# Kernel tuning notes

Measured on AMD Instinct MI355X. Metric: run time of the kernel, lower is better.

Reference implementation:

```python
import jax, jax.numpy as jnp
import numpy as np

B, S, T = 16, 256, 2048
V, D, H, L, FF, NM = 3000, 512, 8, 6, 2048, 80
DH = D // H


def _make_pe(max_len=5000, d=D):
    pos = np.arange(max_len, dtype=np.float32)[:, None]
    div = np.exp(np.arange(0, d, 2, dtype=np.float32) * (-np.log(10000.0) / d))
    pe = np.zeros((max_len, d), dtype=np.float32)
    pe[:, 0::2] = np.sin(pos * div)
    pe[:, 1::2] = np.cos(pos * div)
    return jnp.asarray(pe[None])  # [1, max_len, D]


def setup_inputs() -> dict:
    key = jax.random.key(0)
    ks = jax.random.split(key, 24)
    f = jnp.float32
    n = lambda k, sh, s=0.02: jax.random.normal(k, sh, f) * s
    return {
        'text_ids': jax.random.randint(ks[0], (B, S), 0, V),
        'text_lengths': jax.random.randint(ks[1], (B,), S // 2, S + 1),
        'mel_targets': jax.random.normal(ks[2], (B, NM, T), f),
        'emb': n(ks[3], (V, D), 0.05),
        'pe': _make_pe(),
        'Wqkv': n(ks[4], (L, D, 3 * D)), 'bqkv': jnp.zeros((L, 3 * D), f),
        'Wo': n(ks[5], (L, D, D)), 'bo': jnp.zeros((L, D), f),
        'ln1_s': jnp.ones((L, D), f), 'ln1_b': jnp.zeros((L, D), f),
        'ln2_s': jnp.ones((L, D), f), 'ln2_b': jnp.zeros((L, D), f),
        'W1': n(ks[6], (L, D, FF)), 'b1': jnp.zeros((L, FF), f),
        'W2': n(ks[7], (L, FF, D)), 'b2': jnp.zeros((L, D), f),
        'mel_W1': n(ks[8], (D, FF)), 'mel_b1': jnp.zeros((FF,), f),
        'mel_W2': n(ks[9], (FF, NM)), 'mel_b2': jnp.zeros((NM,), f),
        'dur_W1': n(ks[10], (D, 256)), 'dur_b1': jnp.zeros((256,), f),
        'dur_W2': n(ks[11], (256, 1)), 'dur_b2': jnp.zeros((1,), f),
    }


def _layer_norm(x, s, b, eps=1e-5):
    m = jnp.mean(x, -1, keepdims=True)
    v = jnp.mean(jnp.square(x - m), -1, keepdims=True)
    return (x - m) * jax.lax.rsqrt(v + eps) * s + b


def _length_regulate(enc, durations, target_len):
    # enc [B,S,D], durations [B,S] -> [B,target_len,D]
    dur = jnp.maximum(jnp.round(durations).astype(jnp.int32), 1)
    cum = jnp.cumsum(dur, axis=1)                              # [B,S] inclusive
    pos = jnp.arange(target_len)                               # [T]
    idx = jnp.sum(pos[None, None, :] >= cum[:, :, None], axis=1)  # [B,T]
    idx = jnp.minimum(idx, enc.shape[1] - 1)
    valid = pos[None, :] < cum[:, -1:]                         # [B,T]
    out = jnp.take_along_axis(enc, idx[..., None], axis=1)
    return out * valid[..., None].astype(enc.dtype)


def reference(text_ids, text_lengths, mel_targets, emb, pe, Wqkv, bqkv, Wo, bo,
              ln1_s, ln1_b, ln2_s, ln2_b, W1, b1, W2, b2,
              mel_W1, mel_b1, mel_W2, mel_b2, dur_W1, dur_b1, dur_W2, dur_b2):
    x = emb[text_ids] + pe[:, :S]                              # [B,S,D]
    pad = jnp.arange(S)[None, :] >= text_lengths[:, None]      # True = padded key
    bias = jnp.where(pad, -1e9, 0.0)[:, None, None, :]         # [B,1,1,S]
    scale = 1.0 / jnp.sqrt(jnp.float32(DH))
    for l in range(L):
        qkv = x @ Wqkv[l] + bqkv[l]
        q, k, v = jnp.split(qkv, 3, axis=-1)
        q = q.reshape(B, S, H, DH).transpose(0, 2, 1, 3)
        k = k.reshape(B, S, H, DH).transpose(0, 2, 1, 3)
        v = v.reshape(B, S, H, DH).transpose(0, 2, 1, 3)
        scores = jnp.einsum('bhqd,bhkd->bhqk', q, k) * scale + bias
        attn = jax.nn.softmax(scores, axis=-1)
        o = jnp.einsum('bhqk,bhkd->bhqd', attn, v)
        o = o.transpose(0, 2, 1, 3).reshape(B, S, D) @ Wo[l] + bo[l]
        x = _layer_norm(x + o, ln1_s[l], ln1_b[l])              # post-LN (torch default)
        ff = jax.nn.relu(x @ W1[l] + b1[l]) @ W2[l] + b2[l]
        x = _layer_norm(x + ff, ln2_s[l], ln2_b[l])
    enc = x
    dur_h = jax.nn.relu(enc @ dur_W1 + dur_b1)
    durations = jax.nn.softplus((dur_h @ dur_W2 + dur_b2).squeeze(-1))  # [B,S]
    target_len = mel_targets.shape[2]
    expanded = _length_regulate(enc, durations, target_len)    # [B,T,D]
    mel = jax.nn.relu(expanded @ mel_W1 + mel_b1) @ mel_W2 + mel_b2
    mel = mel.transpose(0, 2, 1)                               # [B,NM,T]
    return mel, durations, enc
```

## Files before the change

### kernel.cpp

```cpp
#include <hip/hip_runtime.h>
#include <math.h>

#define B_ 16
#define S_ 256
#define T_ 2048
#define D_ 512
#define H_ 8
#define L_ 6
#define FF_ 2048
#define NM_ 80
#define M_ 4096

typedef float floatx4 __attribute__((ext_vector_type(4)));
typedef __bf16 bf16x8 __attribute__((ext_vector_type(8)));

__device__ __forceinline__ float bf2f(unsigned u) {
    return __uint_as_float((u & 0xffffu) << 16);
}
__device__ __forceinline__ unsigned short f2bf(float f) {
    unsigned u = __float_as_uint(f);
    unsigned r = u + 0x7fffu + ((u >> 16) & 1u);
    return (unsigned short)(r >> 16);
}
__device__ __forceinline__ void gload_lds16(const void* g, void* l) {
    __builtin_amdgcn_global_load_lds(
        (const __attribute__((address_space(1))) void*)g,
        (__attribute__((address_space(3))) void*)l, 16, 0, 0);
}

__device__ __forceinline__ void tr_body(
    const float* __restrict__ src, unsigned short* __restrict__ dst,
    int K, int N, int bx, int by, int bz, float (*tile)[33], int Ns )
{
    const int k0 = by * 32, n0 = bx * 32;
    src += (size_t)bz * K * Ns;
    dst += (size_t)bz * K * N;
    const int tid = threadIdx.x;
    const int tx = tid & 31, ty = tid >> 5;
#pragma unroll
    for (int i = 0; i < 32; i += 8) {
        int n = n0 + tx;
        tile[ty + i][tx] = (n < Ns) ? src[(size_t)(k0 + ty + i) * Ns + n] : 0.f;
    }
    __syncthreads();
#pragma unroll
    for (int i = 0; i < 32; i += 8)
        dst[(size_t)(n0 + ty + i) * K + k0 + tx] = f2bf(tile[tx][ty + i]);
}

__global__ __launch_bounds__(256) void prep_weights(
    const float* __restrict__ Wqkv, const float* __restrict__ Wo,
    const float* __restrict__ W1, const float* __restrict__ W2,
    const float* __restrict__ melW1, const float* __restrict__ melW2,
    const float* __restrict__ durW1, const float* __restrict__ melb1,
    const float* __restrict__ melb2, const float* __restrict__ durb1,
    unsigned short* __restrict__ Wqkv_t, unsigned short* __restrict__ Wo_t,
    unsigned short* __restrict__ W1_t, unsigned short* __restrict__ W2_t,
    unsigned short* __restrict__ wcomb, unsigned short* __restrict__ melW2_t,
    float* __restrict__ cbias, float* __restrict__ c0)
{
    __shared__ float tile[32][33];
    int bid = blockIdx.x;
    if (bid < 4608) {
        int z = bid / 768, r = bid % 768;
        tr_body(Wqkv, Wqkv_t, 512, 1536, r % 48, r / 48, z, tile, 1536);
        return;
    }
    bid -= 4608;
    if (bid < 1536) {
        int z = bid / 256, r = bid % 256;
        tr_body(Wo, Wo_t, 512, 512, r % 16, r / 16, z, tile, 512);
        return;
    }
    bid -= 1536;
    if (bid < 6144) {
        int z = bid / 1024, r = bid % 1024;
        tr_body(W1, W1_t, 512, 2048, r % 64, r / 64, z, tile, 2048);
        return;
    }
    bid -= 6144;
    if (bid < 6144) {
        int z = bid / 1024, r = bid % 1024;
        tr_body(W2, W2_t, 2048, 512, r % 16, r / 16, z, tile, 512);
        return;
    }
    bid -= 6144;
    if (bid < 1024) {
        tr_body(melW1, wcomb, 512, 2304, bid % 64, bid / 64, 0, tile, 2048);
        return;
    }
    bid -= 1024;
    if (bid < 256) {
        tr_body(melW2, melW2_t, 2048, 128, bid % 4, bid / 4, 0, tile, 80);
        return;
    }
    bid -= 256;
    if (bid < 128) {
        tr_body(durW1, wcomb + (size_t)2048 * 512, 512, 256, bid % 8, bid / 8, 0, tile, 256);
        return;
    }
    bid -= 128;
    if (bid < 9) {
        int idx = bid * 256 + threadIdx.x;
        cbias[idx] = (idx < 2048) ? melb1[idx] : durb1[idx - 2048];
        return;
    }
    bid -= 9;
    {
        float* red = (float*)tile;
        const int c = bid;
        const int tid = threadIdx.x;
        float p = 0.f;
        for (int f = tid; f < 2048; f += 256)
            p += fmaxf(melb1[f], 0.f) * melW2[(size_t)f * 80 + c];
#pragma unroll
        for (int off = 32; off >= 1; off >>= 1) p += __shfl_xor(p, off, 64);
        if ((tid & 63) == 0) red[tid >> 6] = p;
        __syncthreads();
        if (tid == 0) c0[c] = red[0] + red[1] + red[2] + red[3] + melb2[c];
    }
}

__global__ __launch_bounds__(128) void embed_bf16(
    const int* __restrict__ ids, const float* __restrict__ emb,
    const float* __restrict__ pe, unsigned short* __restrict__ x)
{
    const int r = blockIdx.x;
    const int c = threadIdx.x * 4;
    const int id = ids[r];
    const int s = r & (S_ - 1);
    float4 e = *(const float4*)(emb + (size_t)id * D_ + c);
    float4 p = *(const float4*)(pe + (size_t)s * D_ + c);
    ushort4 o;
    o.x = f2bf(e.x + p.x); o.y = f2bf(e.y + p.y);
    o.z = f2bf(e.z + p.z); o.w = f2bf(e.w + p.w);
    *(ushort4*)(x + (size_t)r * D_ + c) = o;
}

template<int BM, int BN>
__global__ __launch_bounds__(256) void gemm2(
    const unsigned short* __restrict__ A, const unsigned short* __restrict__ Bt,
    const float* __restrict__ bias, unsigned short* __restrict__ Cb,
    float* __restrict__ Cpart, unsigned short* __restrict__ vtp,
    int N, int klen, int act, int lda)
{
    constexpr int NSUB_A = BM / 8;
    constexpr int NSUB_B = BN / 8;
    constexpr int NSUB = NSUB_A + NSUB_B;
    constexpr int NL = NSUB / 4;
    constexpr int BUFSZ = NSUB * 1024;
    constexpr int AOFF = NSUB_A * 1024;
    constexpr int WM = BM / 32, WN = BN / 32;
    __shared__ __attribute__((aligned(16))) char smem[2 * BUFSZ];

    const int tid = threadIdx.x;
    const int wave = tid >> 6, lane = tid & 63;
    const int lm = lane & 15, quad = lane >> 4;
    const int wm = wave >> 1, wn = wave & 1;
    const int m0 = blockIdx.y * BM;
    const int n0 = blockIdx.x * BN;
    const int Kfull = klen * gridDim.z;
    const int kb = blockIdx.z * klen;

    floatx4 acc[WM][WN];
#pragma unroll
    for (int i = 0; i < WM; i++)
#pragma unroll
        for (int j = 0; j < WN; j++) acc[i][j] = (floatx4){0.f, 0.f, 0.f, 0.f};

    const unsigned short* ga[NL];
    int loff[NL];
#pragma unroll
    for (int j = 0; j < NL; j++) {
        int sid = wave * NL + j;
        if (sid < NSUB_A) {
            int mi = sid >> 1, ki = sid & 1;
            ga[j] = A + (size_t)(m0 + mi * 16 + lm) * lda + kb + ki * 32 + quad * 8;
            loff[j] = sid * 1024;
        } else {
            int t = sid - NSUB_A;
            int ni = t >> 1, ki = t & 1;
            ga[j] = Bt + (size_t)(n0 + ni * 16 + lm) * Kfull + kb + ki * 32 + quad * 8;
            loff[j] = AOFF + t * 1024;
        }
    }

#pragma unroll
    for (int j = 0; j < NL; j++) gload_lds16(ga[j], smem + loff[j]);

    for (int kt = 0; kt < klen; kt += 64) {
        char* sc = smem + ((kt >> 6) & 1) * BUFSZ;
        if (kt + 64 < klen) {
            char* sn = smem + (((kt >> 6) + 1) & 1) * BUFSZ;
#pragma unroll
            for (int j = 0; j < NL; j++) gload_lds16(ga[j] + kt + 64, sn + loff[j]);
            __builtin_amdgcn_s_waitcnt(0x0F70 | NL);
        } else {
            __builtin_amdgcn_s_waitcnt(0x0F70);
        }
        asm volatile("" ::: "memory");
        __builtin_amdgcn_s_barrier();
        asm volatile("" ::: "memory");

#pragma unroll
        for (int ki = 0; ki < 2; ki++) {
            bf16x8 af[WM], bfr[WN];
#pragma unroll
            for (int i = 0; i < WM; i++)
                af[i] = *(const bf16x8*)(sc + ((((wm * WM + i) * 2 + ki) << 10) + (lane << 4)));
#pragma unroll
            for (int j = 0; j < WN; j++)
                bfr[j] = *(const bf16x8*)(sc + AOFF + ((((wn * WN + j) * 2 + ki) << 10) + (lane << 4)));
#pragma unroll
            for (int i = 0; i < WM; i++)
#pragma unroll
                for (int j = 0; j < WN; j++)
                    acc[i][j] = __builtin_amdgcn_mfma_f32_16x16x32_bf16(
                        af[i], bfr[j], acc[i][j], 0, 0, 0);
        }
        asm volatile("" ::: "memory");
        __builtin_amdgcn_s_barrier();
        asm volatile("" ::: "memory");
    }

    if constexpr (BM == 128 && BN == 128) {
        if (vtp != nullptr && n0 >= 1024) {
            unsigned short* sT = (unsigned short*)smem;
#pragma unroll
            for (int mi = 0; mi < WM; mi++) {
                const int rl = wm * 64 + mi * 16 + quad * 4;
#pragma unroll
                for (int nj = 0; nj < WN; nj++) {
                    const int cl = wn * 64 + nj * 16 + lm;
                    const float bv = bias[n0 + cl];
                    ushort4 t4;
                    t4.x = f2bf(acc[mi][nj][0] + bv);
                    t4.y = f2bf(acc[mi][nj][1] + bv);
                    t4.z = f2bf(acc[mi][nj][2] + bv);
                    t4.w = f2bf(acc[mi][nj][3] + bv);
                    *(ushort4*)(sT + cl * 136 + rl) = t4;
                }
            }
            __syncthreads();
            const int b = m0 >> 8;
            const int s0 = m0 & 255;
            const int h0 = (n0 - 1024) >> 6;
#pragma unroll
            for (int i = 0; i < 8; i++) {
                int idx = i * 256 + tid;
                int d = idx >> 4, c = idx & 15;
                uint4 v = *(const uint4*)(sT + d * 136 + c * 8);
                int bh = b * 8 + h0 + (d >> 6);
                *(uint4*)(vtp + ((size_t)bh * 64 + (d & 63)) * 256 + s0 + c * 8) = v;
            }
            return;
        }
    }

    if (gridDim.z == 1) {
#pragma unroll
        for (int mi = 0; mi < WM; mi++) {
            const int rb = m0 + wm * (WM * 16) + mi * 16 + quad * 4;
#pragma unroll
            for (int nj = 0; nj < WN; nj++) {
                const int col = n0 + wn * (WN * 16) + nj * 16 + lm;
                const float bv = bias[col];
#pragma unroll
                for (int r = 0; r < 4; r++) {
                    float o = acc[mi][nj][r] + bv;
                    if (act) o = fmaxf(o, 0.f);
                    Cb[(size_t)(rb + r) * N + col] = f2bf(o);
                }
            }
        }
    } else {
        float* Cp = Cpart + (size_t)blockIdx.z * gridDim.y * BM * N;
#pragma unroll
        for (int mi = 0; mi < WM; mi++) {
            const int rb = m0 + wm * (WM * 16) + mi * 16 + quad * 4;
#pragma unroll
            for (int nj = 0; nj < WN; nj++) {
                const int col = n0 + wn * (WN * 16) + nj * 16 + lm;
#pragma unroll
                for (int r = 0; r < 4; r++)
                    Cp[(size_t)(rb + r) * N + col] = acc[mi][nj][r];
            }
        }
    }
}

__global__ __launch_bounds__(256) void attn_fused(
    const unsigned short* __restrict__ qkv, const unsigned short* __restrict__ vt,
    const int* __restrict__ lens, unsigned short* __restrict__ o)
{
    __shared__ __attribute__((aligned(16))) char smem[34816];
    const int tid = threadIdx.x;
    const int wave = tid >> 6, lane = tid & 63;
    const int lm = lane & 15, quad = lane >> 4;
    const int qt = blockIdx.x;
    const int bh = blockIdx.y;
    const int b = bh >> 3, h = bh & 7;
    const int len = lens[b];
    const unsigned short* Qb = qkv + ((size_t)b * 256 + qt * 128) * 1536 + h * 64;
    const unsigned short* Kb = qkv + (size_t)b * 256 * 1536 + 512 + h * 64;
    const unsigned short* Vt = vt + (size_t)bh * 64 * 256;

#pragma unroll
    for (int j = 0; j < 8; j++) {
        int sid = wave * 8 + j;
        int nf = sid >> 1, kf = sid & 1;
        gload_lds16(Kb + (size_t)(nf * 16 + lm) * 1536 + kf * 32 + quad * 8,
                    smem + sid * 1024);
    }
    bf16x8 aq[2][2];
#pragma unroll
    for (int mi = 0; mi < 2; mi++)
#pragma unroll
        for (int kf = 0; kf < 2; kf++)
            aq[mi][kf] = *(const bf16x8*)(Qb + (size_t)(wave * 32 + mi * 16 + lm) * 1536
                                          + kf * 32 + quad * 8);
    __syncthreads();

    floatx4 accS[2][16];
#pragma unroll
    for (int mi = 0; mi < 2; mi++)
#pragma unroll
        for (int nf = 0; nf < 16; nf++) accS[mi][nf] = (floatx4){0.f, 0.f, 0.f, 0.f};

#pragma unroll
    for (int nf = 0; nf < 16; nf++) {
        bf16x8 bk0 = *(const bf16x8*)(smem + (nf * 2 + 0) * 1024 + lane * 16);
        bf16x8 bk1 = *(const bf16x8*)(smem + (nf * 2 + 1) * 1024 + lane * 16);
        accS[0][nf] = __builtin_amdgcn_mfma_f32_16x16x32_bf16(aq[0][0], bk0, accS[0][nf], 0, 0, 0);
        accS[0][nf] = __builtin_amdgcn_mfma_f32_16x16x32_bf16(aq[0][1], bk1, accS[0][nf], 0, 0, 0);
        accS[1][nf] = __builtin_amdgcn_mfma_f32_16x16x32_bf16(aq[1][0], bk0, accS[1][nf], 0, 0, 0);
        accS[1][nf] = __builtin_amdgcn_mfma_f32_16x16x32_bf16(aq[1][1], bk1, accS[1][nf], 0, 0, 0);
    }

    float lrow[2][4];
    const float scale = 0.125f;
#pragma unroll
    for (int mi = 0; mi < 2; mi++)
#pragma unroll
        for (int r = 0; r < 4; r++) {
            float sum = 0.f;
#pragma unroll
            for (int nf = 0; nf < 16; nf++) {
                float s = accS[mi][nf][r] * scale + ((nf * 16 + lm >= len) ? -1e9f : 0.f);
                float e = __expf(s);
                accS[mi][nf][r] = e;
                sum += e;
            }
#pragma unroll
            for (int off = 1; off < 16; off <<= 1) sum += __shfl_xor(sum, off, 64);
            lrow[mi][r] = sum;
        }

    floatx4 accO[2][4];
#pragma unroll
    for (int mi = 0; mi < 2; mi++)
#pragma unroll
        for (int nj = 0; nj < 4; nj++) accO[mi][nj] = (floatx4){0.f, 0.f, 0.f, 0.f};

    __syncthreads();
    unsigned short* sP = (unsigned short*)smem;
    const int rbase = wave * 32;
#pragma unroll
    for (int half = 0; half < 2; half++) {
#pragma unroll
        for (int mi = 0; mi < 2; mi++)
#pragma unroll
            for (int nf2 = 0; nf2 < 8; nf2++) {
                int nf = half * 8 + nf2;
                int row = rbase + mi * 16 + quad * 4;
                int col = nf2 * 16 + lm;
#pragma unroll
                for (int r = 0; r < 4; r++)
                    sP[(row + r) * 136 + col] = f2bf(accS[mi][nf][r]);
            }
#pragma unroll
        for (int ks2 = 0; ks2 < 4; ks2++) {
            bf16x8 ap[2];
#pragma unroll
            for (int mi = 0; mi < 2; mi++)
                ap[mi] = *(const bf16x8*)(sP + (rbase + mi * 16 + lm) * 136
                                          + ks2 * 32 + quad * 8);
            int ks = half * 4 + ks2;
#pragma unroll
            for (int nj = 0; nj < 4; nj++) {
                bf16x8 bv = *(const bf16x8*)(Vt + (size_t)(nj * 16 + lm) * 256
                                             + ks * 32 + quad * 8);
                accO[0][nj] = __builtin_amdgcn_mfma_f32_16x16x32_bf16(ap[0], bv, accO[0][nj], 0, 0, 0);
                accO[1][nj] = __builtin_amdgcn_mfma_f32_16x16x32_bf16(ap[1], bv, accO[1][nj], 0, 0, 0);
            }
        }
    }

#pragma unroll
    for (int mi = 0; mi < 2; mi++) {
        float inv[4];
#pragma unroll
        for (int r = 0; r < 4; r++) inv[r] = 1.f / lrow[mi][r];
        const int grow = b * 256 + qt * 128 + rbase + mi * 16 + quad * 4;
#pragma unroll
        for (int nj = 0; nj < 4; nj++) {
            const int gcol = h * 64 + nj * 16 + lm;
#pragma unroll
            for (int r = 0; r < 4; r++)
                o[(size_t)(grow + r) * 512 + gcol] = f2bf(accO[mi][nj][r] * inv[r]);
        }
    }
}

__global__ __launch_bounds__(128) void add_ln_bf16(
    unsigned short* __restrict__ x, const unsigned short* __restrict__ y,
    const float* __restrict__ s, const float* __restrict__ bb)
{
    __shared__ float red[2];
    const int row = blockIdx.x;
    const int tid = threadIdx.x;
    const int c = tid * 4;
    ushort4 xv = *(const ushort4*)(x + (size_t)row * D_ + c);
    ushort4 yv = *(const ushort4*)(y + (size_t)row * D_ + c);
    float h[4];
    h[0] = bf2f(xv.x) + bf2f(yv.x);
    h[1] = bf2f(xv.y) + bf2f(yv.y);
    h[2] = bf2f(xv.z) + bf2f(yv.z);
    h[3] = bf2f(xv.w) + bf2f(yv.w);

    float sum = h[0] + h[1] + h[2] + h[3];
#pragma unroll
    for (int off = 32; off >= 1; off >>= 1) sum += __shfl_xor(sum, off, 64);
    if ((tid & 63) == 0) red[tid >> 6] = sum;
    __syncthreads();
    float mean = (red[0] + red[1]) * (1.f / 512.f);
    __syncthreads();

    float d[4];
    d[0] = h[0] - mean; d[1] = h[1] - mean; d[2] = h[2] - mean; d[3] = h[3] - mean;
    float sq = d[0] * d[0] + d[1] * d[1] + d[2] * d[2] + d[3] * d[3];
#pragma unroll
    for (int off = 32; off >= 1; off >>= 1) sq += __shfl_xor(sq, off, 64);
    if ((tid & 63) == 0) red[tid >> 6] = sq;
    __syncthreads();
    float var = (red[0] + red[1]) * (1.f / 512.f);
    float rs = rsqrtf(var + 1e-5f);

    float4 sv = *(const float4*)(s + c);
    float4 bv = *(const float4*)(bb + c);
    ushort4 ov;
    ov.x = f2bf(d[0] * rs * sv.x + bv.x);
    ov.y = f2bf(d[1] * rs * sv.y + bv.y);
    ov.z = f2bf(d[2] * rs * sv.z + bv.z);
    ov.w = f2bf(d[3] * rs * sv.w + bv.w);
    *(ushort4*)(x + (size_t)row * D_ + c) = ov;
}

__global__ __launch_bounds__(128) void add_ln_part(
    unsigned short* __restrict__ x, const float* __restrict__ p0,
    const float* __restrict__ p1, const float* __restrict__ bias,
    const float* __restrict__ s, const float* __restrict__ bb,
    float* __restrict__ enc_opt)
{
    __shared__ float red[2];
    const int row = blockIdx.x;
    const int tid = threadIdx.x;
    const int c = tid * 4;
    ushort4 xv = *(const ushort4*)(x + (size_t)row * D_ + c);
    float4 a = *(const float4*)(p0 + (size_t)row * D_ + c);
    float4 bq = *(const float4*)(p1 + (size_t)row * D_ + c);
    float4 bi = *(const float4*)(bias + c);
    float h[4];
    h[0] = bf2f(xv.x) + a.x + bq.x + bi.x;
    h[1] = bf2f(xv.y) + a.y + bq.y + bi.y;
    h[2] = bf2f(xv.z) + a.z + bq.z + bi.z;
    h[3] = bf2f(xv.w) + a.w + bq.w + bi.w;

    float sum = h[0] + h[1] + h[2] + h[3];
#pragma unroll
    for (int off = 32; off >= 1; off >>= 1) sum += __shfl_xor(sum, off, 64);
    if ((tid & 63) == 0) red[tid >> 6] = sum;
    __syncthreads();
    float mean = (red[0] + red[1]) * (1.f / 512.f);
    __syncthreads();

    float d[4];
    d[0] = h[0] - mean; d[1] = h[1] - mean; d[2] = h[2] - mean; d[3] = h[3] - mean;
    float sq = d[0] * d[0] + d[1] * d[1] + d[2] * d[2] + d[3] * d[3];
#pragma unroll
    for (int off = 32; off >= 1; off >>= 1) sq += __shfl_xor(sq, off, 64);
    if ((tid & 63) == 0) red[tid >> 6] = sq;
    __syncthreads();
    float var = (red[0] + red[1]) * (1.f / 512.f);
    float rs = rsqrtf(var + 1e-5f);

    float4 sv = *(const float4*)(s + c);
    float4 bv = *(const float4*)(bb + c);
    float o[4];
    o[0] = d[0] * rs * sv.x + bv.x;
    o[1] = d[1] * rs * sv.y + bv.y;
    o[2] = d[2] * rs * sv.z + bv.z;
    o[3] = d[3] * rs * sv.w + bv.w;
    ushort4 ov;
    ov.x = f2bf(o[0]); ov.y = f2bf(o[1]); ov.z = f2bf(o[2]); ov.w = f2bf(o[3]);
    *(ushort4*)(x + (size_t)row * D_ + c) = ov;
    if (enc_opt) {
        float4 e; e.x = o[0]; e.y = o[1]; e.z = o[2]; e.w = o[3];
        *(float4*)(enc_opt + (size_t)row * D_ + c) = e;
    }
}

__global__ __launch_bounds__(256) void dur_rows(
    const unsigned short* __restrict__ hcomb, const float* __restrict__ w2,
    const float* __restrict__ b2, float* __restrict__ durout,
    int* __restrict__ dint)
{
    const int tid = threadIdx.x;
    const int w = tid >> 6, lane = tid & 63;
    const int r = blockIdx.x * 4 + w;
    ushort4 hv = *(const ushort4*)(hcomb + (size_t)r * 2304 + 2048 + lane * 4);
    float4 wv = *(const float4*)(w2 + lane * 4);
    float p = bf2f(hv.x) * wv.x + bf2f(hv.y) * wv.y
            + bf2f(hv.z) * wv.z + bf2f(hv.w) * wv.w;
#pragma unroll
    for (int off = 32; off >= 1; off >>= 1) p += __shfl_xor(p, off, 64);
    if (lane == 0) {
        float v = p + b2[0];
        float dur = (v > 20.f) ? v : log1pf(expf(v));
        durout[r] = dur;
        int d = (int)rintf(dur);
        if (d < 1) d = 1;
        dint[r] = d;
    }
}

__global__ __launch_bounds__(256) void dur_scan(
    const int* __restrict__ dint, int* __restrict__ cum)
{
    __shared__ int sd[256];
    const int tid = threadIdx.x;
    const int b = blockIdx.x;
    sd[tid] = dint[b * 256 + tid];
    __syncthreads();
    for (int off = 1; off < 256; off <<= 1) {
        int v = sd[tid];
        int add = (tid >= off) ? sd[tid - off] : 0;
        __syncthreads();
        sd[tid] = v + add;
        __syncthreads();
    }
    cum[b * 256 + tid] = sd[tid];
}

__global__ __launch_bounds__(256) void mel_combine(
    const float* __restrict__ mp, const float* __restrict__ b2,
    float* __restrict__ melc)
{
    const int idx = blockIdx.x * 256 + threadIdx.x;
    const int r = idx / 80, c = idx - r * 80;
    const size_t plane = (size_t)M_ * 128;
    const size_t base = (size_t)r * 128 + c;
    melc[idx] = mp[base] + mp[plane + base] + mp[2 * plane + base]
              + mp[3 * plane + base] + b2[c];
}

__global__ __launch_bounds__(256) void mel_gather2(
    const float* __restrict__ melc, const float* __restrict__ c0,
    const int* __restrict__ cum, float* __restrict__ mel_out)
{
    __shared__ float rows[256 * 40];
    __shared__ int sc[256];
    __shared__ float s0[40];
    const int tid = threadIdx.x;
    const int b = blockIdx.z;
    const int cc0 = blockIdx.y * 40;
    sc[tid] = cum[b * 256 + tid];
    if (tid < 40) s0[tid] = c0[cc0 + tid];
    for (int idx = tid; idx < 256 * 40; idx += 256) {
        int r = idx / 40, c = idx - r * 40;
        rows[idx] = melc[((size_t)b * 256 + r) * 80 + cc0 + c];
    }
    __syncthreads();
    const int total = sc[255];
    const int t = blockIdx.x * 256 + tid;
    int lo = 0, hi = 256;
    while (lo < hi) {
        int mid = (lo + hi) >> 1;
        if (sc[mid] <= t) lo = mid + 1; else hi = mid;
    }
    int row = lo < 255 ? lo : 255;
    const bool valid = t < total;
    const float* src = valid ? &rows[row * 40] : s0;
    for (int cc = 0; cc < 40; cc++)
        mel_out[((size_t)b * 80 + cc0 + cc) * T_ + t] = src[cc];
}

extern "C" void kernel_launch(void* const* d_in, const int* in_sizes, int n_in,
                              void* d_out, int out_size, void* d_ws, size_t ws_size,
                              hipStream_t stream)
{
    const int*   text_ids     = (const int*)d_in[0];
    const int*   text_lengths = (const int*)d_in[1];
    const float* emb   = (const float*)d_in[3];
    const float* pe    = (const float*)d_in[4];
    const float* Wqkv  = (const float*)d_in[5];
    const float* bqkv  = (const float*)d_in[6];
    const float* Wo    = (const float*)d_in[7];
    const float* bo    = (const float*)d_in[8];
    const float* ln1_s = (const float*)d_in[9];
    const float* ln1_b = (const float*)d_in[10];
    const float* ln2_s = (const float*)d_in[11];
    const float* ln2_b = (const float*)d_in[12];
    const float* W1    = (const float*)d_in[13];
    const float* b1    = (const float*)d_in[14];
    const float* W2    = (const float*)d_in[15];
    const float* b2    = (const float*)d_in[16];
    const float* mel_W1 = (const float*)d_in[17];
    const float* mel_b1 = (const float*)d_in[18];
    const float* mel_W2 = (const float*)d_in[19];
    const float* mel_b2 = (const float*)d_in[20];
    const float* dur_W1 = (const float*)d_in[21];
    const float* dur_b1 = (const float*)d_in[22];
    const float* dur_W2 = (const float*)d_in[23];
    const float* dur_b2 = (const float*)d_in[24];

    float* out = (float*)d_out;
    float* mel_out = out;
    float* dur_out = out + (size_t)B_ * NM_ * T_;
    float* enc_out = dur_out + (size_t)B_ * S_;

    typedef unsigned short u16;
    char* w = (char*)d_ws;
    u16* Wqkv_t  = (u16*)w;                   w += (size_t)L_ * 1536 * 512 * 2;
    u16* Wo_t    = (u16*)w;                   w += (size_t)L_ * 512 * 512 * 2;
    u16* W1_t    = (u16*)w;                   w += (size_t)L_ * 2048 * 512 * 2;
    u16* W2_t    = (u16*)w;                   w += (size_t)L_ * 512 * 2048 * 2;
    u16* wcomb   = (u16*)w;                   w += (size_t)2304 * 512 * 2;
    u16* melW2_t = (u16*)w;                   w += (size_t)128 * 2048 * 2;
    u16* x_bf    = (u16*)w;                   w += (size_t)M_ * 512 * 2;
    u16* qkv_bf  = (u16*)w;                   w += (size_t)M_ * 1536 * 2;
    u16* ao_bf   = (u16*)w;                   w += (size_t)M_ * 512 * 2;
    u16* y_bf    = (u16*)w;                   w += (size_t)M_ * 512 * 2;
    char* big    = w;                         w += (size_t)18874368;
    float* c0    = (float*)w;                 w += 512;
    int*   cum   = (int*)w;                   w += (size_t)M_ * 4;
    int*   dint  = (int*)w;                   w += (size_t)M_ * 4;
    float* cbias = (float*)w;                 w += (size_t)2304 * 4;
    float* melc  = (float*)w;                 w += (size_t)M_ * 80 * 4;

    u16* ffh     = (u16*)big;
    u16* hcomb   = (u16*)big;
    u16* vt      = (u16*)(big + 12582912);

    float* part2 = (float*)qkv_bf;
    float* mpart = (float*)(qkv_bf + (size_t)M_ * 512);

    prep_weights<<<19929, 256, 0, stream>>>(
        Wqkv, Wo, W1, W2, mel_W1, mel_W2, dur_W1, mel_b1, mel_b2, dur_b1,
        Wqkv_t, Wo_t, W1_t, W2_t, wcomb, melW2_t, cbias, c0);

    embed_bf16<<<M_, 128, 0, stream>>>(text_ids, emb, pe, x_bf);

    for (int l = 0; l < L_; l++) {
        gemm2<128, 128><<<dim3(12, 32), 256, 0, stream>>>(
            x_bf, Wqkv_t + (size_t)l * 1536 * 512, bqkv + (size_t)l * 1536,
            qkv_bf, nullptr, vt, 1536, 512, 0, 512);
        attn_fused<<<dim3(2, 128), 256, 0, stream>>>(qkv_bf, vt, text_lengths, ao_bf);
        gemm2<128, 64><<<dim3(8, 32), 256, 0, stream>>>(
            ao_bf, Wo_t + (size_t)l * 512 * 512, bo + (size_t)l * 512,
            y_bf, nullptr, nullptr, 512, 512, 0, 512);
        add_ln_bf16<<<M_, 128, 0, stream>>>(
            x_bf, y_bf, ln1_s + (size_t)l * D_, ln1_b + (size_t)l * D_);
        gemm2<128, 128><<<dim3(16, 32), 256, 0, stream>>>(
            x_bf, W1_t + (size_t)l * 2048 * 512, b1 + (size_t)l * 2048,
            ffh, nullptr, nullptr, 2048, 512, 1, 512);
        gemm2<128, 64><<<dim3(8, 32, 2), 256, 0, stream>>>(
            ffh, W2_t + (size_t)l * 512 * 2048, nullptr,
            nullptr, part2, nullptr, 512, 1024, 0, 2048);
        add_ln_part<<<M_, 128, 0, stream>>>(
            x_bf, part2, part2 + (size_t)M_ * 512, b2 + (size_t)l * 512,
            ln2_s + (size_t)l * D_, ln2_b + (size_t)l * D_,
            (l == L_ - 1) ? enc_out : nullptr);
    }

    gemm2<128, 128><<<dim3(18, 32), 256, 0, stream>>>(
        x_bf, wcomb, cbias, hcomb, nullptr, nullptr, 2304, 512, 1, 512);

    dur_rows<<<M_ / 4, 256, 0, stream>>>(hcomb, dur_W2, dur_b2, dur_out, dint);
    dur_scan<<<B_, 256, 0, stream>>>(dint, cum);

    gemm2<128, 64><<<dim3(2, 32, 4), 256, 0, stream>>>(
        hcomb, melW2_t, nullptr, nullptr, mpart, nullptr, 128, 512, 0, 2304);
    mel_combine<<<1280, 256, 0, stream>>>(mpart, mel_b2, melc);
    mel_gather2<<<dim3(T_ / 256, 2, B_), 256, 0, stream>>>(melc, c0, cum, mel_out);
}
```

Before: 837.3 us.

## Retile attention per wave, remap GEMM blocks across XCDs, widen layernorm rows

The attention kernel now runs one 64-thread wave per 16 query rows and reads K directly from global memory instead of staging it in LDS. This launches 2048 small blocks in place of 256 large ones, aiming for better occupancy at the cost of repeated K loads. The GEMM remaps block indices so that neighbouring tiles land on the same XCD for L2 reuse, and moves its wait and barrier to after each compute step. The layernorm kernels now process one row per wave with 8-element vectors, removing the shared-memory reductions. Weight transposes are written as packed 32-bit stores.

```diff
diff --git a/kernel.cpp b/kernel.cpp
--- a/kernel.cpp
+++ b/kernel.cpp
@@ -13,6 +13,7 @@
 
 typedef float floatx4 __attribute__((ext_vector_type(4)));
 typedef __bf16 bf16x8 __attribute__((ext_vector_type(8)));
+typedef unsigned short u16x8 __attribute__((ext_vector_type(8)));
 
 __device__ __forceinline__ float bf2f(unsigned u) {
     return __uint_as_float((u & 0xffffu) << 16);
@@ -43,9 +44,13 @@
         tile[ty + i][tx] = (n < Ns) ? src[(size_t)(k0 + ty + i) * Ns + n] : 0.f;
     }
     __syncthreads();
-#pragma unroll
-    for (int i = 0; i < 32; i += 8)
-        dst[(size_t)(n0 + ty + i) * K + k0 + tx] = f2bf(tile[tx][ty + i]);
+    const int tx2 = tid & 15, ty2 = tid >> 4;
+#pragma unroll
+    for (int i = 0; i < 32; i += 16) {
+        unsigned lo = f2bf(tile[2 * tx2][ty2 + i]);
+        unsigned hi = f2bf(tile[2 * tx2 + 1][ty2 + i]);
+        *(unsigned*)(dst + (size_t)(n0 + ty2 + i) * K + k0 + 2 * tx2) = lo | (hi << 16);
+    }
 }
 
 __global__ __launch_bounds__(256) void prep_weights(
@@ -157,8 +162,15 @@
     const int wave = tid >> 6, lane = tid & 63;
     const int lm = lane & 15, quad = lane >> 4;
     const int wm = wave >> 1, wn = wave & 1;
-    const int m0 = blockIdx.y * BM;
-    const int n0 = blockIdx.x * BN;
+
+    const int gx = gridDim.x;
+    const int nwg = gx * gridDim.y;
+    const int flat = blockIdx.y * gx + blockIdx.x;
+    const int qc = nwg >> 3, rc = nwg & 7;
+    const int xcd = flat & 7, off = flat >> 3;
+    const int wg = (xcd < rc ? xcd * (qc + 1) : rc * (qc + 1) + (xcd - rc) * qc) + off;
+    const int m0 = (wg / gx) * BM;
+    const int n0 = (wg % gx) * BN;
     const int Kfull = klen * gridDim.z;
     const int kb = blockIdx.z * klen;
 
@@ -187,6 +199,10 @@
 
 #pragma unroll
     for (int j = 0; j < NL; j++) gload_lds16(ga[j], smem + loff[j]);
+    __builtin_amdgcn_s_waitcnt(0x0F70);
+    asm volatile("" ::: "memory");
+    __builtin_amdgcn_s_barrier();
+    asm volatile("" ::: "memory");
 
     for (int kt = 0; kt < klen; kt += 64) {
         char* sc = smem + ((kt >> 6) & 1) * BUFSZ;
@@ -194,13 +210,7 @@
             char* sn = smem + (((kt >> 6) + 1) & 1) * BUFSZ;
 #pragma unroll
             for (int j = 0; j < NL; j++) gload_lds16(ga[j] + kt + 64, sn + loff[j]);
-            __builtin_amdgcn_s_waitcnt(0x0F70 | NL);
-        } else {
-            __builtin_amdgcn_s_waitcnt(0x0F70);
-        }
-        asm volatile("" ::: "memory");
-        __builtin_amdgcn_s_barrier();
-        asm volatile("" ::: "memory");
+        }
 
 #pragma unroll
         for (int ki = 0; ki < 2; ki++) {
@@ -219,6 +229,7 @@
                         af[i], bfr[j], acc[i][j], 0, 0, 0);
         }
         asm volatile("" ::: "memory");
+        __builtin_amdgcn_s_waitcnt(0x0F70);
         __builtin_amdgcn_s_barrier();
         asm volatile("" ::: "memory");
     }
@@ -289,224 +300,198 @@
     }
 }
 
-__global__ __launch_bounds__(256) void attn_fused(
+__global__ __launch_bounds__(64) void attn_fused(
     const unsigned short* __restrict__ qkv, const unsigned short* __restrict__ vt,
     const int* __restrict__ lens, unsigned short* __restrict__ o)
 {
-    __shared__ __attribute__((aligned(16))) char smem[34816];
-    const int tid = threadIdx.x;
-    const int wave = tid >> 6, lane = tid & 63;
+    __shared__ __attribute__((aligned(16))) unsigned short sP[16 * 280];
+    const int lane = threadIdx.x;
     const int lm = lane & 15, quad = lane >> 4;
     const int qt = blockIdx.x;
     const int bh = blockIdx.y;
     const int b = bh >> 3, h = bh & 7;
     const int len = lens[b];
-    const unsigned short* Qb = qkv + ((size_t)b * 256 + qt * 128) * 1536 + h * 64;
+    const unsigned short* Qb = qkv + ((size_t)b * 256 + qt * 16) * 1536 + h * 64;
     const unsigned short* Kb = qkv + (size_t)b * 256 * 1536 + 512 + h * 64;
     const unsigned short* Vt = vt + (size_t)bh * 64 * 256;
 
-#pragma unroll
-    for (int j = 0; j < 8; j++) {
-        int sid = wave * 8 + j;
-        int nf = sid >> 1, kf = sid & 1;
-        gload_lds16(Kb + (size_t)(nf * 16 + lm) * 1536 + kf * 32 + quad * 8,
-                    smem + sid * 1024);
-    }
-    bf16x8 aq[2][2];
-#pragma unroll
-    for (int mi = 0; mi < 2; mi++)
-#pragma unroll
-        for (int kf = 0; kf < 2; kf++)
-            aq[mi][kf] = *(const bf16x8*)(Qb + (size_t)(wave * 32 + mi * 16 + lm) * 1536
-                                          + kf * 32 + quad * 8);
-    __syncthreads();
-
-    floatx4 accS[2][16];
-#pragma unroll
-    for (int mi = 0; mi < 2; mi++)
-#pragma unroll
-        for (int nf = 0; nf < 16; nf++) accS[mi][nf] = (floatx4){0.f, 0.f, 0.f, 0.f};
+    bf16x8 aq0 = *(const bf16x8*)(Qb + (size_t)lm * 1536 + quad * 8);
+    bf16x8 aq1 = *(const bf16x8*)(Qb + (size_t)lm * 1536 + 32 + quad * 8);
+
+    floatx4 accS[16];
+#pragma unroll
+    for (int nf = 0; nf < 16; nf++) accS[nf] = (floatx4){0.f, 0.f, 0.f, 0.f};
 
 #pragma unroll
     for (int nf = 0; nf < 16; nf++) {
-        bf16x8 bk0 = *(const bf16x8*)(smem + (nf * 2 + 0) * 1024 + lane * 16);
-        bf16x8 bk1 = *(const bf16x8*)(smem + (nf * 2 + 1) * 1024 + lane * 16);
-        accS[0][nf] = __builtin_amdgcn_mfma_f32_16x16x32_bf16(aq[0][0], bk0, accS[0][nf], 0, 0, 0);
-        accS[0][nf] = __builtin_amdgcn_mfma_f32_16x16x32_bf16(aq[0][1], bk1, accS[0][nf], 0, 0, 0);
-        accS[1][nf] = __builtin_amdgcn_mfma_f32_16x16x32_bf16(aq[1][0], bk0, accS[1][nf], 0, 0, 0);
-        accS[1][nf] = __builtin_amdgcn_mfma_f32_16x16x32_bf16(aq[1][1], bk1, accS[1][nf], 0, 0, 0);
-    }
-
-    float lrow[2][4];
+        const unsigned short* kr = Kb + (size_t)(nf * 16 + lm) * 1536 + quad * 8;
+        bf16x8 bk0 = *(const bf16x8*)(kr);
+        bf16x8 bk1 = *(const bf16x8*)(kr + 32);
+        accS[nf] = __builtin_amdgcn_mfma_f32_16x16x32_bf16(aq0, bk0, accS[nf], 0, 0, 0);
+        accS[nf] = __builtin_amdgcn_mfma_f32_16x16x32_bf16(aq1, bk1, accS[nf], 0, 0, 0);
+    }
+
+    float lrow[4];
     const float scale = 0.125f;
 #pragma unroll
-    for (int mi = 0; mi < 2; mi++)
-#pragma unroll
-        for (int r = 0; r < 4; r++) {
-            float sum = 0.f;
-#pragma unroll
-            for (int nf = 0; nf < 16; nf++) {
-                float s = accS[mi][nf][r] * scale + ((nf * 16 + lm >= len) ? -1e9f : 0.f);
-                float e = __expf(s);
-                accS[mi][nf][r] = e;
-                sum += e;
-            }
-#pragma unroll
-            for (int off = 1; off < 16; off <<= 1) sum += __shfl_xor(sum, off, 64);
-            lrow[mi][r] = sum;
-        }
-
-    floatx4 accO[2][4];
-#pragma unroll
-    for (int mi = 0; mi < 2; mi++)
-#pragma unroll
-        for (int nj = 0; nj < 4; nj++) accO[mi][nj] = (floatx4){0.f, 0.f, 0.f, 0.f};
-
-    __syncthreads();
-    unsigned short* sP = (unsigned short*)smem;
-    const int rbase = wave * 32;
-#pragma unroll
-    for (int half = 0; half < 2; half++) {
-#pragma unroll
-        for (int mi = 0; mi < 2; mi++)
-#pragma unroll
-            for (int nf2 = 0; nf2 < 8; nf2++) {
-                int nf = half * 8 + nf2;
-                int row = rbase + mi * 16 + quad * 4;
-                int col = nf2 * 16 + lm;
-#pragma unroll
-                for (int r = 0; r < 4; r++)
-                    sP[(row + r) * 136 + col] = f2bf(accS[mi][nf][r]);
-            }
-#pragma unroll
-        for (int ks2 = 0; ks2 < 4; ks2++) {
-            bf16x8 ap[2];
-#pragma unroll
-            for (int mi = 0; mi < 2; mi++)
-                ap[mi] = *(const bf16x8*)(sP + (rbase + mi * 16 + lm) * 136
-                                          + ks2 * 32 + quad * 8);
-            int ks = half * 4 + ks2;
-#pragma unroll
-            for (int nj = 0; nj < 4; nj++) {
-                bf16x8 bv = *(const bf16x8*)(Vt + (size_t)(nj * 16 + lm) * 256
-                                             + ks * 32 + quad * 8);
-                accO[0][nj] = __builtin_amdgcn_mfma_f32_16x16x32_bf16(ap[0], bv, accO[0][nj], 0, 0, 0);
-                accO[1][nj] = __builtin_amdgcn_mfma_f32_16x16x32_bf16(ap[1], bv, accO[1][nj], 0, 0, 0);
-            }
-        }
-    }
-
-#pragma unroll
-    for (int mi = 0; mi < 2; mi++) {
-        float inv[4];
-#pragma unroll
-        for (int r = 0; r < 4; r++) inv[r] = 1.f / lrow[mi][r];
-        const int grow = b * 256 + qt * 128 + rbase + mi * 16 + quad * 4;
+    for (int r = 0; r < 4; r++) {
+        float sum = 0.f;
+#pragma unroll
+        for (int nf = 0; nf < 16; nf++) {
+            float s = accS[nf][r] * scale + ((nf * 16 + lm >= len) ? -1e9f : 0.f);
+            float e = __expf(s);
+            accS[nf][r] = e;
+            sum += e;
+        }
+#pragma unroll
+        for (int off = 1; off < 16; off <<= 1) sum += __shfl_xor(sum, off, 64);
+        lrow[r] = sum;
+    }
+
+#pragma unroll
+    for (int nf = 0; nf < 16; nf++) {
+        const int col = nf * 16 + lm;
+#pragma unroll
+        for (int r = 0; r < 4; r++)
+            sP[(quad * 4 + r) * 280 + col] = f2bf(accS[nf][r]);
+    }
+
+    floatx4 accO[4];
+#pragma unroll
+    for (int nj = 0; nj < 4; nj++) accO[nj] = (floatx4){0.f, 0.f, 0.f, 0.f};
+
+#pragma unroll
+    for (int ks = 0; ks < 8; ks++) {
+        bf16x8 ap = *(const bf16x8*)(sP + lm * 280 + ks * 32 + quad * 8);
 #pragma unroll
         for (int nj = 0; nj < 4; nj++) {
-            const int gcol = h * 64 + nj * 16 + lm;
-#pragma unroll
-            for (int r = 0; r < 4; r++)
-                o[(size_t)(grow + r) * 512 + gcol] = f2bf(accO[mi][nj][r] * inv[r]);
-        }
-    }
-}
-
-__global__ __launch_bounds__(128) void add_ln_bf16(
+            bf16x8 bv = *(const bf16x8*)(Vt + (size_t)(nj * 16 + lm) * 256
+                                         + ks * 32 + quad * 8);
+            accO[nj] = __builtin_amdgcn_mfma_f32_16x16x32_bf16(ap, bv, accO[nj], 0, 0, 0);
+        }
+    }
+
+    float inv[4];
+#pragma unroll
+    for (int r = 0; r < 4; r++) inv[r] = 1.f / lrow[r];
+    const int grow = b * 256 + qt * 16 + quad * 4;
+#pragma unroll
+    for (int nj = 0; nj < 4; nj++) {
+        const int gcol = h * 64 + nj * 16 + lm;
+#pragma unroll
+        for (int r = 0; r < 4; r++)
+            o[(size_t)(grow + r) * 512 + gcol] = f2bf(accO[nj][r] * inv[r]);
+    }
+}
+
+__global__ __launch_bounds__(512) void add_ln_bf16(
     unsigned short* __restrict__ x, const unsigned short* __restrict__ y,
     const float* __restrict__ s, const float* __restrict__ bb)
 {
-    __shared__ float red[2];
-    const int row = blockIdx.x;
-    const int tid = threadIdx.x;
-    const int c = tid * 4;
-    ushort4 xv = *(const ushort4*)(x + (size_t)row * D_ + c);
-    ushort4 yv = *(const ushort4*)(y + (size_t)row * D_ + c);
-    float h[4];
-    h[0] = bf2f(xv.x) + bf2f(yv.x);
-    h[1] = bf2f(xv.y) + bf2f(yv.y);
-    h[2] = bf2f(xv.z) + bf2f(yv.z);
-    h[3] = bf2f(xv.w) + bf2f(yv.w);
-
-    float sum = h[0] + h[1] + h[2] + h[3];
+    const int wave = threadIdx.x >> 6, lane = threadIdx.x & 63;
+    const int row = blockIdx.x * 8 + wave;
+    const int c = lane * 8;
+    u16x8 xv = *(const u16x8*)(x + (size_t)row * D_ + c);
+    u16x8 yv = *(const u16x8*)(y + (size_t)row * D_ + c);
+    float h[8];
+    float sum = 0.f;
+#pragma unroll
+    for (int j = 0; j < 8; j++) {
+        h[j] = bf2f(xv[j]) + bf2f(yv[j]);
+        sum += h[j];
+    }
 #pragma unroll
     for (int off = 32; off >= 1; off >>= 1) sum += __shfl_xor(sum, off, 64);
-    if ((tid & 63) == 0) red[tid >> 6] = sum;
-    __syncthreads();
-    float mean = (red[0] + red[1]) * (1.f / 512.f);
-    __syncthreads();
-
-    float d[4];
-    d[0] = h[0] - mean; d[1] = h[1] - mean; d[2] = h[2] - mean; d[3] = h[3] - mean;
-    float sq = d[0] * d[0] + d[1] * d[1] + d[2] * d[2] + d[3] * d[3];
+    float mean = sum * (1.f / 512.f);
+
+    float d[8], sq = 0.f;
+#pragma unroll
+    for (int j = 0; j < 8; j++) {
+        d[j] = h[j] - mean;
+        sq += d[j] * d[j];
+    }
 #pragma unroll
     for (int off = 32; off >= 1; off >>= 1) sq += __shfl_xor(sq, off, 64);
-    if ((tid & 63) == 0) red[tid >> 6] = sq;
-    __syncthreads();
-    float var = (red[0] + red[1]) * (1.f / 512.f);
-    float rs = rsqrtf(var + 1e-5f);
-
-    float4 sv = *(const float4*)(s + c);
-    float4 bv = *(const float4*)(bb + c);
-    ushort4 ov;
-    ov.x = f2bf(d[0] * rs * sv.x + bv.x);
-    ov.y = f2bf(d[1] * rs * sv.y + bv.y);
-    ov.z = f2bf(d[2] * rs * sv.z + bv.z);
-    ov.w = f2bf(d[3] * rs * sv.w + bv.w);
-    *(ushort4*)(x + (size_t)row * D_ + c) = ov;
-}
-
-__global__ __launch_bounds__(128) void add_ln_part(
+    float rs = rsqrtf(sq * (1.f / 512.f) + 1e-5f);
+
+    float4 sv0 = *(const float4*)(s + c), sv1 = *(const float4*)(s + c + 4);
+    float4 bv0 = *(const float4*)(bb + c), bv1 = *(const float4*)(bb + c + 4);
+    u16x8 ov;
+    ov[0] = f2bf(d[0] * rs * sv0.x + bv0.x);
+    ov[1] = f2bf(d[1] * rs * sv0.y + bv0.y);
+    ov[2] = f2bf(d[2] * rs * sv0.z + bv0.z);
+    ov[3] = f2bf(d[3] * rs * sv0.w + bv0.w);
+    ov[4] = f2bf(d[4] * rs * sv1.x + bv1.x);
+    ov[5] = f2bf(d[5] * rs * sv1.y + bv1.y);
+    ov[6] = f2bf(d[6] * rs * sv1.z + bv1.z);
+    ov[7] = f2bf(d[7] * rs * sv1.w + bv1.w);
+    *(u16x8*)(x + (size_t)row * D_ + c) = ov;
+}
+
+__global__ __launch_bounds__(512) void add_ln_part(
     unsigned short* __restrict__ x, const float* __restrict__ p0,
     const float* __restrict__ p1, const float* __restrict__ bias,
     const float* __restrict__ s, const float* __restrict__ bb,
     float* __restrict__ enc_opt)
 {
-    __shared__ float red[2];
-    const int row = blockIdx.x;
-    const int tid = threadIdx.x;
-    const int c = tid * 4;
-    ushort4 xv = *(const ushort4*)(x + (size_t)row * D_ + c);
-    float4 a = *(const float4*)(p0 + (size_t)row * D_ + c);
-    float4 bq = *(const float4*)(p1 + (size_t)row * D_ + c);
-    float4 bi = *(const float4*)(bias + c);
-    float h[4];
-    h[0] = bf2f(xv.x) + a.x + bq.x + bi.x;
-    h[1] = bf2f(xv.y) + a.y + bq.y + bi.y;
-    h[2] = bf2f(xv.z) + a.z + bq.z + bi.z;
-    h[3] = bf2f(xv.w) + a.w + bq.w + bi.w;
-
-    float sum = h[0] + h[1] + h[2] + h[3];
+    const int wave = threadIdx.x >> 6, lane = threadIdx.x & 63;
+    const int row = blockIdx.x * 8 + wave;
+    const int c = lane * 8;
+    u16x8 xv = *(const u16x8*)(x + (size_t)row * D_ + c);
+    float4 a0 = *(const float4*)(p0 + (size_t)row * D_ + c);
+    float4 a1 = *(const float4*)(p0 + (size_t)row * D_ + c + 4);
+    float4 q0 = *(const float4*)(p1 + (size_t)row * D_ + c);
+    float4 q1 = *(const float4*)(p1 + (size_t)row * D_ + c + 4);
+    float4 bi0 = *(const float4*)(bias + c);
+    float4 bi1 = *(const float4*)(bias + c + 4);
+    float h[8];
+    h[0] = bf2f(xv[0]) + a0.x + q0.x + bi0.x;
+    h[1] = bf2f(xv[1]) + a0.y + q0.y + bi0.y;
+    h[2] = bf2f(xv[2]) + a0.z + q0.z + bi0.z;
+    h[3] = bf2f(xv[3]) + a0.w + q0.w + bi0.w;
+    h[4] = bf2f(xv[4]) + a1.x + q1.x + bi1.x;
+    h[5] = bf2f(xv[5]) + a1.y + q1.y + bi1.y;
+    h[6] = bf2f(xv[6]) + a1.z + q1.z + bi1.z;
+    h[7] = bf2f(xv[7]) + a1.w + q1.w + bi1.w;
+
+    float sum = 0.f;
+#pragma unroll
+    for (int j = 0; j < 8; j++) sum += h[j];
 #pragma unroll
     for (int off = 32; off >= 1; off >>= 1) sum += __shfl_xor(sum, off, 64);
-    if ((tid & 63) == 0) red[tid >> 6] = sum;
-    __syncthreads();
-    float mean = (red[0] + red[1]) * (1.f / 512.f);
-    __syncthreads();
-
-    float d[4];
-    d[0] = h[0] - mean; d[1] = h[1] - mean; d[2] = h[2] - mean; d[3] = h[3] - mean;
-    float sq = d[0] * d[0] + d[1] * d[1] + d[2] * d[2] + d[3] * d[3];
+    float mean = sum * (1.f / 512.f);
+
+    float d[8], sq = 0.f;
+#pragma unroll
+    for (int j = 0; j < 8; j++) {
+        d[j] = h[j] - mean;
+        sq += d[j] * d[j];
+    }
 #pragma unroll
     for (int off = 32; off >= 1; off >>= 1) sq += __shfl_xor(sq, off, 64);
-    if ((tid & 63) == 0) red[tid >> 6] = sq;
-    __syncthreads();
-    float var = (red[0] + red[1]) * (1.f / 512.f);
-    float rs = rsqrtf(var + 1e-5f);
-
-    float4 sv = *(const float4*)(s + c);
-    float4 bv = *(const float4*)(bb + c);
-    float o[4];
-    o[0] = d[0] * rs * sv.x + bv.x;
-    o[1] = d[1] * rs * sv.y + bv.y;
-    o[2] = d[2] * rs * sv.z + bv.z;
-    o[3] = d[3] * rs * sv.w + bv.w;
-    ushort4 ov;
-    ov.x = f2bf(o[0]); ov.y = f2bf(o[1]); ov.z = f2bf(o[2]); ov.w = f2bf(o[3]);
-    *(ushort4*)(x + (size_t)row * D_ + c) = ov;
+    float rs = rsqrtf(sq * (1.f / 512.f) + 1e-5f);
+
+    float4 sv0 = *(const float4*)(s + c), sv1 = *(const float4*)(s + c + 4);
+    float4 bv0 = *(const float4*)(bb + c), bv1 = *(const float4*)(bb + c + 4);
+    float o[8];
+    o[0] = d[0] * rs * sv0.x + bv0.x;
+    o[1] = d[1] * rs * sv0.y + bv0.y;
+    o[2] = d[2] * rs * sv0.z + bv0.z;
+    o[3] = d[3] * rs * sv0.w + bv0.w;
+    o[4] = d[4] * rs * sv1.x + bv1.x;
+    o[5] = d[5] * rs * sv1.y + bv1.y;
+    o[6] = d[6] * rs * sv1.z + bv1.z;
+    o[7] = d[7] * rs * sv1.w + bv1.w;
+    u16x8 ov;
+#pragma unroll
+    for (int j = 0; j < 8; j++) ov[j] = f2bf(o[j]);
+    *(u16x8*)(x + (size_t)row * D_ + c) = ov;
     if (enc_opt) {
-        float4 e; e.x = o[0]; e.y = o[1]; e.z = o[2]; e.w = o[3];
-        *(float4*)(enc_opt + (size_t)row * D_ + c) = e;
+        float4 e0, e1;
+        e0.x = o[0]; e0.y = o[1]; e0.z = o[2]; e0.w = o[3];
+        e1.x = o[4]; e1.y = o[5]; e1.z = o[6]; e1.w = o[7];
+        *(float4*)(enc_opt + (size_t)row * D_ + c) = e0;
+        *(float4*)(enc_opt + (size_t)row * D_ + c + 4) = e1;
     }
 }
 
@@ -665,11 +650,11 @@
         gemm2<128, 128><<<dim3(12, 32), 256, 0, stream>>>(
             x_bf, Wqkv_t + (size_t)l * 1536 * 512, bqkv + (size_t)l * 1536,
             qkv_bf, nullptr, vt, 1536, 512, 0, 512);
-        attn_fused<<<dim3(2, 128), 256, 0, stream>>>(qkv_bf, vt, text_lengths, ao_bf);
+        attn_fused<<<dim3(16, 128), 64, 0, stream>>>(qkv_bf, vt, text_lengths, ao_bf);
         gemm2<128, 64><<<dim3(8, 32), 256, 0, stream>>>(
             ao_bf, Wo_t + (size_t)l * 512 * 512, bo + (size_t)l * 512,
             y_bf, nullptr, nullptr, 512, 512, 0, 512);
-        add_ln_bf16<<<M_, 128, 0, stream>>>(
+        add_ln_bf16<<<M_ / 8, 512, 0, stream>>>(
             x_bf, y_bf, ln1_s + (size_t)l * D_, ln1_b + (size_t)l * D_);
         gemm2<128, 128><<<dim3(16, 32), 256, 0, stream>>>(
             x_bf, W1_t + (size_t)l * 2048 * 512, b1 + (size_t)l * 2048,
@@ -677,7 +662,7 @@
         gemm2<128, 64><<<dim3(8, 32, 2), 256, 0, stream>>>(
             ffh, W2_t + (size_t)l * 512 * 2048, nullptr,
             nullptr, part2, nullptr, 512, 1024, 0, 2048);
-        add_ln_part<<<M_, 128, 0, stream>>>(
+        add_ln_part<<<M_ / 8, 512, 0, stream>>>(
             x_bf, part2, part2 + (size_t)M_ * 512, b2 + (size_t)l * 512,
             ln2_s + (size_t)l * D_, ln2_b + (size_t)l * D_,
             (l == L_ - 1) ? enc_out : nullptr);
```

Result: slower. 897.2 us (+7.2%).
